# Optimization experiments

Measured on AMD Instinct MI355X. Metric: run time of the kernel, lower is better.

## Reference

```python
import jax, jax.numpy as jnp
import numpy as np

N_ATOMS = 524288
N_FEAT = 128
BATCH_SIZE = 16384


def setup_inputs() -> dict:
    key = jax.random.key(0)
    k1, k2 = jax.random.split(key)
    atom_features = jax.random.normal(k1, (N_ATOMS, N_FEAT), dtype=jnp.float32)
    membership = jnp.sort(
        jax.random.randint(k2, (N_ATOMS,), 0, BATCH_SIZE, dtype=jnp.int32)
    )
    return {
        "atom_features": atom_features,
        "membership": membership,
        "batch_size": BATCH_SIZE,
    }


def reference(atom_features, membership, batch_size):
    # Fused equivalent of dynamic_partition + per-segment reduce_sum + concat:
    # a single segment-sum keyed on membership. Activation is 'linear' (identity).
    mol_features = jax.ops.segment_sum(
        atom_features, membership, num_segments=batch_size
    )  # (batch_size, n_feat)
    return mol_features
```

## Files before the change

kernel.cpp:

```cpp
#include <hip/hip_runtime.h>

#define N_FEAT 128
#define F4_PER_ROW (N_FEAT / 4)

__global__ __launch_bounds__(64) void seg_sum_kernel(
    const float* __restrict__ feats,
    const int* __restrict__ membership,
    float* __restrict__ out,
    int n_atoms)
{
    const int seg  = blockIdx.x;
    const int lane = threadIdx.x;

    int res = 0;
    if (lane < 2) {
        const int target = seg + lane;
        int l = 0, r = n_atoms;
        while (l < r) {
            int m = (l + r) >> 1;
            if (membership[m] < target) l = m + 1; else r = m;
        }
        res = l;
    }
    const int lo = __shfl(res, 0);
    const int hi = __shfl(res, 1);

    const int tx = lane & 31;
    const int ty = lane >> 5;

    float4 acc = make_float4(0.f, 0.f, 0.f, 0.f);
    const float4* __restrict__ f4 = (const float4*)feats;

    for (int r = lo + ty; r < hi; r += 2) {
        float4 v = f4[r * F4_PER_ROW + tx];
        acc.x += v.x; acc.y += v.y; acc.z += v.z; acc.w += v.w;
    }

    acc.x += __shfl_down(acc.x, 32);
    acc.y += __shfl_down(acc.y, 32);
    acc.z += __shfl_down(acc.z, 32);
    acc.w += __shfl_down(acc.w, 32);

    if (ty == 0) {
        ((float4*)out)[seg * F4_PER_ROW + tx] = acc;
    }
}

extern "C" void kernel_launch(void* const* d_in, const int* in_sizes, int n_in,
                              void* d_out, int out_size, void* d_ws, size_t ws_size,
                              hipStream_t stream) {
    const float* feats      = (const float*)d_in[0];
    const int*   membership = (const int*)d_in[1];
    float*       out        = (float*)d_out;

    const int n_atoms = in_sizes[1];
    const int batch   = out_size / N_FEAT;

    seg_sum_kernel<<<batch, 64, 0, stream>>>(feats, membership, out, n_atoms);
}
```

Baseline: 375.9 us.

## Precompute segment starts in separate kernel and unroll nontemporal loads in segment sum

Replaces the per-block binary search over membership with a pre-pass kernel that writes segment start offsets into workspace. The sum kernel then packs four segments per 256-thread block and unrolls the row loop into four independent accumulators fed by nontemporal loads. The goal is more memory-level parallelism and less search latency, at the cost of an extra kernel launch and a workspace buffer. Empty segments at the start are handled by the scatter loop.

```diff
diff --git a/kernel.cpp b/kernel.cpp
--- a/kernel.cpp
+++ b/kernel.cpp
@@ -1,40 +1,64 @@
 #include <hip/hip_runtime.h>
 
 #define N_FEAT 128
-#define F4_PER_ROW (N_FEAT / 4)
+#define F4 (N_FEAT / 4)
+#define SEGS_PER_BLOCK 4
 
-__global__ __launch_bounds__(64) void seg_sum_kernel(
+typedef float vfloat4 __attribute__((ext_vector_type(4)));
+
+__global__ __launch_bounds__(256) void seg_starts_kernel(
+    const int* __restrict__ membership, int* __restrict__ starts, int n_atoms,
+    int batch)
+{
+    int i = blockIdx.x * blockDim.x + threadIdx.x;
+    if (i >= n_atoms) return;
+    int cur  = membership[i];
+    int prev = (i == 0) ? -1 : membership[i - 1];
+    for (int s = prev + 1; s <= cur; ++s) starts[s] = i;
+    if (i == n_atoms - 1) {
+        for (int s = cur + 1; s <= batch; ++s) starts[s] = n_atoms;
+    }
+}
+
+__global__ __launch_bounds__(256) void seg_sum_kernel(
     const float* __restrict__ feats,
-    const int* __restrict__ membership,
+    const int* __restrict__ starts,
     float* __restrict__ out,
-    int n_atoms)
+    int batch)
 {
-    const int seg  = blockIdx.x;
-    const int lane = threadIdx.x;
+    const int wave = threadIdx.x >> 6;
+    const int lane = threadIdx.x & 63;
+    const int seg  = blockIdx.x * SEGS_PER_BLOCK + wave;
+    if (seg >= batch) return;
 
-    int res = 0;
-    if (lane < 2) {
-        const int target = seg + lane;
-        int l = 0, r = n_atoms;
-        while (l < r) {
-            int m = (l + r) >> 1;
-            if (membership[m] < target) l = m + 1; else r = m;
-        }
-        res = l;
-    }
-    const int lo = __shfl(res, 0);
-    const int hi = __shfl(res, 1);
+    const int lo = starts[seg];
+    const int hi = starts[seg + 1];
 
     const int tx = lane & 31;
     const int ty = lane >> 5;
 
-    float4 acc = make_float4(0.f, 0.f, 0.f, 0.f);
-    const float4* __restrict__ f4 = (const float4*)feats;
+    const vfloat4* __restrict__ f4 = (const vfloat4*)feats;
 
-    for (int r = lo + ty; r < hi; r += 2) {
-        float4 v = f4[r * F4_PER_ROW + tx];
-        acc.x += v.x; acc.y += v.y; acc.z += v.z; acc.w += v.w;
+    vfloat4 a0 = {0.f, 0.f, 0.f, 0.f};
+    vfloat4 a1 = a0, a2 = a0, a3 = a0;
+
+    int r = lo + ty;
+    for (; r + 6 < hi; r += 8) {
+        const vfloat4* p = f4 + r * F4 + tx;
+        vfloat4 v0 = __builtin_nontemporal_load(p);
+        vfloat4 v1 = __builtin_nontemporal_load(p + 2 * F4);
+        vfloat4 v2 = __builtin_nontemporal_load(p + 4 * F4);
+        vfloat4 v3 = __builtin_nontemporal_load(p + 6 * F4);
+        a0 += v0;
+        a1 += v1;
+        a2 += v2;
+        a3 += v3;
     }
+    for (; r < hi; r += 2) {
+        a0 += __builtin_nontemporal_load(f4 + r * F4 + tx);
+    }
+
+    vfloat4 acc = (a0 + a1) + (a2 + a3);
 
     acc.x += __shfl_down(acc.x, 32);
     acc.y += __shfl_down(acc.y, 32);
@@ -42,7 +66,7 @@
     acc.w += __shfl_down(acc.w, 32);
 
     if (ty == 0) {
-        ((float4*)out)[seg * F4_PER_ROW + tx] = acc;
+        ((vfloat4*)out)[seg * F4 + tx] = acc;
     }
 }
 
@@ -52,9 +76,14 @@
     const float* feats      = (const float*)d_in[0];
     const int*   membership = (const int*)d_in[1];
     float*       out        = (float*)d_out;
+    int*         starts     = (int*)d_ws;
 
     const int n_atoms = in_sizes[1];
     const int batch   = out_size / N_FEAT;
 
-    seg_sum_kernel<<<batch, 64, 0, stream>>>(feats, membership, out, n_atoms);
+    seg_starts_kernel<<<(n_atoms + 255) / 256, 256, 0, stream>>>(
+        membership, starts, n_atoms, batch);
+
+    seg_sum_kernel<<<(batch + SEGS_PER_BLOCK - 1) / SEGS_PER_BLOCK, 256, 0,
+                     stream>>>(feats, starts, out, batch);
 }
```

Result: faster. 341.3 us (median of 2 runs) (-9.2%).
